# Kernel tuning notes

Hardware: AMD Instinct MI355X
Metric: run time of the kernel (lower is better)

Reference implementation:

```python
import jax, jax.numpy as jnp
import numpy as np

DX = 1.0 / 126.0  # grid spacing (code uses dx for both x and y derivatives)
CN_MAX = 0.1


def _rep_pad(x):
    # replicate-pad last two dims by 1 (torch F.pad mode='replicate')
    return jnp.pad(x, ((0, 0), (0, 0), (1, 1), (1, 1)), mode='edge')


def setup_inputs() -> dict:
    key = jax.random.key(0)
    inputs = jax.random.normal(key, (16, 4, 1024, 1024), dtype=jnp.float32)
    return {"inputs": inputs}


def reference(inputs):
    dx = jnp.asarray(DX, dtype=inputs.dtype)
    u = inputs[:, 0:1]
    v = inputs[:, 1:2]
    T_prev = inputs[:, 2:3]
    RaQ_Ra = inputs[:, 3:4]

    Tp = _rep_pad(T_prev)  # [B,1,H+2,W+2]
    c = Tp[..., 1:-1, 1:-1]  # center == T_prev
    # upwind first differences (torch conv kernels: dx_left=[-1,1,0], dx_right=[0,-1,1], etc.)
    dT_dx_l = (c - Tp[..., 1:-1, :-2]) / dx   # backward diff in x
    dT_dx_r = (Tp[..., 1:-1, 2:] - c) / dx    # forward diff in x
    dT_dy_t = (c - Tp[..., :-2, 1:-1]) / dx   # backward diff in y (original divides by dx)
    dT_dy_b = (Tp[..., 2:, 1:-1] - c) / dx    # forward diff in y

    dT_dx = dT_dx_l * (u > 0) + dT_dx_r * (u < 0)
    dT_dy = dT_dy_t * (v > 0) + dT_dy_b * (v < 0)

    # CFL timestep
    uv_mag = jnp.maximum(jnp.max(jnp.abs(u)), jnp.max(jnp.abs(v)))
    dt_advect = 0.5 * CN_MAX * dx / uv_mag
    dt_diffuse = 0.5 * (dx * dx) ** 2 / (dx ** 2 + dx ** 2)
    dt = jnp.minimum(dt_advect, dt_diffuse)

    # advection step
    T_new = T_prev + dt * (-u * dT_dx - v * dT_dy)

    # diffusion step with 9-point laplacian: 0.25*[[1,2,1],[2,-12,2],[1,2,1]]
    Tp2 = _rep_pad(T_new)
    lap = 0.25 * (
        Tp2[..., :-2, :-2] + 2.0 * Tp2[..., :-2, 1:-1] + Tp2[..., :-2, 2:]
        + 2.0 * Tp2[..., 1:-1, :-2] - 12.0 * Tp2[..., 1:-1, 1:-1] + 2.0 * Tp2[..., 1:-1, 2:]
        + Tp2[..., 2:, :-2] + 2.0 * Tp2[..., 2:, 1:-1] + Tp2[..., 2:, 2:]
    ) / (dx ** 2)
    T_new = T_new + dt * (lap + RaQ_Ra)
    return (T_new, dt)
```

## Files before the change

### kernel.cpp

```cpp
#include <hip/hip_runtime.h>

constexpr int NB = 16;
constexpr int NH = 1024;
constexpr int NW = 1024;

constexpr int TX = 64;
constexpr int TY = 16;
constexpr int SW  = TX + 5;
constexpr int SNW = TX + 3;

__global__ __launch_bounds__(256) void uvmax_kernel(const float4* __restrict__ in,
                                                    unsigned int* __restrict__ outbits) {
    const size_t n4 = (size_t)NB * 2 * NH * NW / 4;
    size_t tid = (size_t)blockIdx.x * blockDim.x + threadIdx.x;
    size_t stride = (size_t)gridDim.x * blockDim.x;
    float m = 0.0f;
    for (size_t i = tid; i < n4; i += stride) {
        size_t b   = i >> 19;
        size_t off = i & ((1u << 19) - 1);
        float4 x = in[b * (1u << 20) + off];
        m = fmaxf(m, fmaxf(fmaxf(fabsf(x.x), fabsf(x.y)),
                           fmaxf(fabsf(x.z), fabsf(x.w))));
    }
    for (int o = 32; o > 0; o >>= 1) m = fmaxf(m, __shfl_down(m, o));
    __shared__ float sm[4];
    int lane = threadIdx.x & 63, wave = threadIdx.x >> 6;
    if (lane == 0) sm[wave] = m;
    __syncthreads();
    if (threadIdx.x == 0) {
        float mm = fmaxf(fmaxf(sm[0], sm[1]), fmaxf(sm[2], sm[3]));
        atomicMax(outbits, __float_as_uint(mm));
    }
}

__global__ __launch_bounds__(256) void step_kernel(const float* __restrict__ in,
                                                   const unsigned int* __restrict__ maxbits,
                                                   float* __restrict__ out) {
    __shared__ float sT[(TY + 4) * SW];
    __shared__ float sN[(TY + 2) * SNW];

    const int b  = blockIdx.z;
    const int x0 = blockIdx.x * TX;
    const int y0 = blockIdx.y * TY;

    const size_t cs = (size_t)NH * NW;
    const float* Uc = in + (size_t)b * 4 * cs;
    const float* Vc = Uc + cs;
    const float* Tc = Uc + 2 * cs;
    const float* Rc = Uc + 3 * cs;

    const float dx  = 1.0f / 126.0f;
    const float dx2 = dx * dx;
    const float uv_mag = __uint_as_float(*maxbits);
    const float dt_adv = 0.5f * 0.1f * dx / uv_mag;
    const float dt_dif = 0.5f * (dx2 * dx2) / (dx2 + dx2);
    const float dt = fminf(dt_adv, dt_dif);

    const int tid = threadIdx.x;

    for (int idx = tid; idx < (TY + 4) * (TX + 4); idx += 256) {
        int j = idx / (TX + 4);
        int i = idx - j * (TX + 4);
        int gy = min(max(y0 + j - 2, 0), NH - 1);
        int gx = min(max(x0 + i - 2, 0), NW - 1);
        sT[j * SW + i] = Tc[(size_t)gy * NW + gx];
    }
    __syncthreads();

    for (int idx = tid; idx < (TY + 2) * (TX + 2); idx += 256) {
        int ty = idx / (TX + 2);
        int tx = idx - ty * (TX + 2);
        int gy = y0 + ty - 1, gx = x0 + tx - 1;
        int cgy = min(max(gy, 0), NH - 1);
        int cgx = min(max(gx, 0), NW - 1);
        int lj = cgy - y0 + 2;
        int li = cgx - x0 + 2;
        float c  = sT[lj * SW + li];
        float lf = sT[lj * SW + li - 1];
        float rt = sT[lj * SW + li + 1];
        float tp = sT[(lj - 1) * SW + li];
        float bt = sT[(lj + 1) * SW + li];
        float u = Uc[(size_t)cgy * NW + cgx];
        float v = Vc[(size_t)cgy * NW + cgx];
        float dT_dx = (u > 0.0f) ? (c - lf) / dx : ((u < 0.0f) ? (rt - c) / dx : 0.0f);
        float dT_dy = (v > 0.0f) ? (c - tp) / dx : ((v < 0.0f) ? (bt - c) / dx : 0.0f);
        sN[ty * SNW + tx] = c + dt * (-u * dT_dx - v * dT_dy);
    }
    __syncthreads();

    float* Ob = out + (size_t)b * cs;
    for (int idx = tid; idx < TY * TX; idx += 256) {
        int ty = idx / TX;
        int tx = idx - ty * TX;
        int gy = y0 + ty, gx = x0 + tx;
        const float* r0 = &sN[ty * SNW + tx];
        const float* r1 = r0 + SNW;
        const float* r2 = r1 + SNW;
        float lap = 0.25f * (r0[0] + 2.0f * r0[1] + r0[2]
                           + 2.0f * r1[0] - 12.0f * r1[1] + 2.0f * r1[2]
                           + r2[0] + 2.0f * r2[1] + r2[2]) / dx2;
        Ob[(size_t)gy * NW + gx] = r1[1] + dt * (lap + Rc[(size_t)gy * NW + gx]);
    }

    if (b == 0 && blockIdx.x == 0 && blockIdx.y == 0 && tid == 0) {
        out[(size_t)NB * cs] = dt;
    }
}

extern "C" void kernel_launch(void* const* d_in, const int* in_sizes, int n_in,
                              void* d_out, int out_size, void* d_ws, size_t ws_size,
                              hipStream_t stream) {
    const float* in = (const float*)d_in[0];
    float* out = (float*)d_out;
    unsigned int* maxbits = (unsigned int*)d_ws;

    hipMemsetAsync(d_ws, 0, sizeof(unsigned int), stream);

    uvmax_kernel<<<1024, 256, 0, stream>>>((const float4*)in, maxbits);

    dim3 grid(NW / TX, NH / TY, NB);
    step_kernel<<<grid, 256, 0, stream>>>(in, maxbits, out);
}
```

Measured before the change: 431.5 us.

## Vectorize stencil loads/stores, enlarge tiles, replace atomic max with partial reduction

Reworks the stencil kernel to load T, u, v and RaQ and store outputs as float4, with tiles enlarged to 128x32 so halo overhead per output shrinks. The global atomicMax and memset are replaced by per-block partial maxima that every step block reduces itself from 1024 partials, which removes the memset launch. Divisions are folded into precomputed constants. Each thread now handles four columns with more shared-memory traffic per thread, and every block repeats the small reduction over 1024 partials.

```diff
diff --git a/kernel.cpp b/kernel.cpp
--- a/kernel.cpp
+++ b/kernel.cpp
@@ -4,107 +4,154 @@
 constexpr int NH = 1024;
 constexpr int NW = 1024;
 
-constexpr int TX = 64;
-constexpr int TY = 16;
-constexpr int SW  = TX + 5;
-constexpr int SNW = TX + 3;
+constexpr int TX = 128;
+constexpr int TY = 32;
+constexpr int NPART = 1024;
+
+constexpr int RA  = TY + 4;
+constexpr int CA  = TX + 8;
+constexpr int CA4 = CA / 4;
+constexpr int STW = CA + 4;
+constexpr int RB  = TY + 2;
+constexpr int SNW = 140;
 
 __global__ __launch_bounds__(256) void uvmax_kernel(const float4* __restrict__ in,
-                                                    unsigned int* __restrict__ outbits) {
+                                                    float* __restrict__ part) {
     const size_t n4 = (size_t)NB * 2 * NH * NW / 4;
-    size_t tid = (size_t)blockIdx.x * blockDim.x + threadIdx.x;
+    size_t i0 = (size_t)blockIdx.x * blockDim.x + threadIdx.x;
     size_t stride = (size_t)gridDim.x * blockDim.x;
     float m = 0.0f;
-    for (size_t i = tid; i < n4; i += stride) {
+    for (size_t i = i0; i < n4; i += stride) {
         size_t b   = i >> 19;
         size_t off = i & ((1u << 19) - 1);
-        float4 x = in[b * (1u << 20) + off];
+        float4 x = in[(b << 20) + off];
         m = fmaxf(m, fmaxf(fmaxf(fabsf(x.x), fabsf(x.y)),
                            fmaxf(fabsf(x.z), fabsf(x.w))));
     }
     for (int o = 32; o > 0; o >>= 1) m = fmaxf(m, __shfl_down(m, o));
     __shared__ float sm[4];
-    int lane = threadIdx.x & 63, wave = threadIdx.x >> 6;
-    if (lane == 0) sm[wave] = m;
+    if ((threadIdx.x & 63) == 0) sm[threadIdx.x >> 6] = m;
     __syncthreads();
-    if (threadIdx.x == 0) {
-        float mm = fmaxf(fmaxf(sm[0], sm[1]), fmaxf(sm[2], sm[3]));
-        atomicMax(outbits, __float_as_uint(mm));
-    }
+    if (threadIdx.x == 0)
+        part[blockIdx.x] = fmaxf(fmaxf(sm[0], sm[1]), fmaxf(sm[2], sm[3]));
 }
 
 __global__ __launch_bounds__(256) void step_kernel(const float* __restrict__ in,
-                                                   const unsigned int* __restrict__ maxbits,
+                                                   const float* __restrict__ part,
                                                    float* __restrict__ out) {
-    __shared__ float sT[(TY + 4) * SW];
-    __shared__ float sN[(TY + 2) * SNW];
+    __shared__ float sT[RA * STW];
+    __shared__ float sN[RB * SNW];
+    __shared__ float sred[4];
+    __shared__ float sdt;
+
+    const int tid = threadIdx.x;
+
+    {
+        float4 p = ((const float4*)part)[tid];
+        float m = fmaxf(fmaxf(p.x, p.y), fmaxf(p.z, p.w));
+        for (int o = 32; o > 0; o >>= 1) m = fmaxf(m, __shfl_down(m, o));
+        if ((tid & 63) == 0) sred[tid >> 6] = m;
+        __syncthreads();
+        if (tid == 0) {
+            float mm = fmaxf(fmaxf(sred[0], sred[1]), fmaxf(sred[2], sred[3]));
+            const float dx = 1.0f / 126.0f, dx2 = dx * dx;
+            float dta = 0.5f * 0.1f * dx / mm;
+            float dtd = 0.5f * (dx2 * dx2) / (dx2 + dx2);
+            sdt = fminf(dta, dtd);
+        }
+        __syncthreads();
+    }
+    const float dt = sdt;
 
     const int b  = blockIdx.z;
     const int x0 = blockIdx.x * TX;
     const int y0 = blockIdx.y * TY;
-
     const size_t cs = (size_t)NH * NW;
     const float* Uc = in + (size_t)b * 4 * cs;
     const float* Vc = Uc + cs;
     const float* Tc = Uc + 2 * cs;
     const float* Rc = Uc + 3 * cs;
 
-    const float dx  = 1.0f / 126.0f;
-    const float dx2 = dx * dx;
-    const float uv_mag = __uint_as_float(*maxbits);
-    const float dt_adv = 0.5f * 0.1f * dx / uv_mag;
-    const float dt_dif = 0.5f * (dx2 * dx2) / (dx2 + dx2);
-    const float dt = fminf(dt_adv, dt_dif);
+    const float dx    = 1.0f / 126.0f;
+    const float dt_dx = dt / dx;
+    const float q_dx2 = 0.25f / (dx * dx);
 
-    const int tid = threadIdx.x;
-
-    for (int idx = tid; idx < (TY + 4) * (TX + 4); idx += 256) {
-        int j = idx / (TX + 4);
-        int i = idx - j * (TX + 4);
-        int gy = min(max(y0 + j - 2, 0), NH - 1);
-        int gx = min(max(x0 + i - 2, 0), NW - 1);
-        sT[j * SW + i] = Tc[(size_t)gy * NW + gx];
+    for (int idx = tid; idx < RA * CA4; idx += 256) {
+        int j  = idx / CA4;
+        int cc = idx - j * CA4;
+        int gy  = min(max(y0 + j - 2, 0), NH - 1);
+        int gxb = x0 - 4 + 4 * cc;
+        float4 t4;
+        if (gxb >= 0 && gxb + 3 < NW) {
+            t4 = *(const float4*)&Tc[(size_t)gy * NW + gxb];
+        } else {
+            float* f = (float*)&t4;
+            #pragma unroll
+            for (int k = 0; k < 4; k++) {
+                int cgx = min(max(gxb + k, 0), NW - 1);
+                f[k] = Tc[(size_t)gy * NW + cgx];
+            }
+        }
+        *(float4*)&sT[j * STW + 4 * cc] = t4;
     }
     __syncthreads();
 
-    for (int idx = tid; idx < (TY + 2) * (TX + 2); idx += 256) {
-        int ty = idx / (TX + 2);
-        int tx = idx - ty * (TX + 2);
-        int gy = y0 + ty - 1, gx = x0 + tx - 1;
+    for (int idx = tid; idx < RB * CA4; idx += 256) {
+        int ty = idx / CA4;
+        int cc = idx - ty * CA4;
+        int gy  = y0 + ty - 1;
         int cgy = min(max(gy, 0), NH - 1);
-        int cgx = min(max(gx, 0), NW - 1);
-        int lj = cgy - y0 + 2;
-        int li = cgx - x0 + 2;
-        float c  = sT[lj * SW + li];
-        float lf = sT[lj * SW + li - 1];
-        float rt = sT[lj * SW + li + 1];
-        float tp = sT[(lj - 1) * SW + li];
-        float bt = sT[(lj + 1) * SW + li];
-        float u = Uc[(size_t)cgy * NW + cgx];
-        float v = Vc[(size_t)cgy * NW + cgx];
-        float dT_dx = (u > 0.0f) ? (c - lf) / dx : ((u < 0.0f) ? (rt - c) / dx : 0.0f);
-        float dT_dy = (v > 0.0f) ? (c - tp) / dx : ((v < 0.0f) ? (bt - c) / dx : 0.0f);
-        sN[ty * SNW + tx] = c + dt * (-u * dT_dx - v * dT_dy);
+        int lj  = cgy - y0 + 2;
+        int gxb = x0 - 4 + 4 * cc;
+        size_t rowo = (size_t)cgy * NW;
+        bool vec = (gxb >= 0 && gxb + 3 < NW);
+        float4 u4, v4;
+        if (vec) {
+            u4 = *(const float4*)&Uc[rowo + gxb];
+            v4 = *(const float4*)&Vc[rowo + gxb];
+        }
+        float tn[4];
+        #pragma unroll
+        for (int k = 0; k < 4; k++) {
+            int cgx = min(max(gxb + k, 0), NW - 1);
+            float uu = vec ? ((const float*)&u4)[k] : Uc[rowo + cgx];
+            float vv = vec ? ((const float*)&v4)[k] : Vc[rowo + cgx];
+            int li = cgx - x0 + 4;
+            const float* s = &sT[lj * STW + li];
+            float c = s[0];
+            float selx = (uu > 0.f) ? (c - s[-1])
+                       : ((uu < 0.f) ? (s[1] - c) : 0.f);
+            float sely = (vv > 0.f) ? (c - s[-STW])
+                       : ((vv < 0.f) ? (s[STW] - c) : 0.f);
+            tn[k] = c - dt_dx * (uu * selx + vv * sely);
+        }
+        *(float4*)&sN[ty * SNW + 4 * cc] = make_float4(tn[0], tn[1], tn[2], tn[3]);
     }
     __syncthreads();
 
-    float* Ob = out + (size_t)b * cs;
-    for (int idx = tid; idx < TY * TX; idx += 256) {
-        int ty = idx / TX;
-        int tx = idx - ty * TX;
-        int gy = y0 + ty, gx = x0 + tx;
-        const float* r0 = &sN[ty * SNW + tx];
+    float* Ob = out + b * cs;
+    for (int idx = tid; idx < TY * (TX / 4); idx += 256) {
+        int ty = idx / (TX / 4);
+        int cc = idx - ty * (TX / 4);
+        int gy  = y0 + ty;
+        int gxb = x0 + 4 * cc;
+        const float* r0 = &sN[ty * SNW + 4 + 4 * cc];
         const float* r1 = r0 + SNW;
         const float* r2 = r1 + SNW;
-        float lap = 0.25f * (r0[0] + 2.0f * r0[1] + r0[2]
-                           + 2.0f * r1[0] - 12.0f * r1[1] + 2.0f * r1[2]
-                           + r2[0] + 2.0f * r2[1] + r2[2]) / dx2;
-        Ob[(size_t)gy * NW + gx] = r1[1] + dt * (lap + Rc[(size_t)gy * NW + gx]);
+        float4 rq = *(const float4*)&Rc[(size_t)gy * NW + gxb];
+        float o[4];
+        #pragma unroll
+        for (int k = 0; k < 4; k++) {
+            float lap = (        r0[k - 1] + 2.f * r0[k] +        r0[k + 1]
+                        + 2.f * r1[k - 1] - 12.f * r1[k] + 2.f * r1[k + 1]
+                        +       r2[k - 1] + 2.f * r2[k] +        r2[k + 1]) * q_dx2;
+            o[k] = r1[k] + dt * (lap + ((const float*)&rq)[k]);
+        }
+        *(float4*)&Ob[(size_t)gy * NW + gxb] = make_float4(o[0], o[1], o[2], o[3]);
     }
 
-    if (b == 0 && blockIdx.x == 0 && blockIdx.y == 0 && tid == 0) {
+    if (b == 0 && blockIdx.x == 0 && blockIdx.y == 0 && tid == 0)
         out[(size_t)NB * cs] = dt;
-    }
 }
 
 extern "C" void kernel_launch(void* const* d_in, const int* in_sizes, int n_in,
@@ -112,12 +159,10 @@
                               hipStream_t stream) {
     const float* in = (const float*)d_in[0];
     float* out = (float*)d_out;
-    unsigned int* maxbits = (unsigned int*)d_ws;
+    float* part = (float*)d_ws;
 
-    hipMemsetAsync(d_ws, 0, sizeof(unsigned int), stream);
-
-    uvmax_kernel<<<1024, 256, 0, stream>>>((const float4*)in, maxbits);
+    uvmax_kernel<<<NPART, 256, 0, stream>>>((const float4*)in, part);
 
     dim3 grid(NW / TX, NH / TY, NB);
-    step_kernel<<<grid, 256, 0, stream>>>(in, maxbits, out);
+    step_kernel<<<grid, 256, 0, stream>>>(in, part, out);
 }
```

Measured after the change: 421.9 us. -2.2%, faster.
